# Performance work log

Measured on AMD Instinct MI355X. Metric: run time of the kernel, lower is better.

Reference implementation:

```python
import jax, jax.numpy as jnp
import numpy as np

N = 20000          # num nodes
DEG = 8            # directed avg degree before symmetrization
IN_C, HID, OUT_C, K = 128, 32, 16, 2


def _build_graph(n, deg, seed=0):
    """Build symmetric 1-hop A1 (no self loops) and exact 2-hop A2 edge lists,
    with D^{-1/2} A D^{-1/2} normalized values (mirrors _prepare_prop)."""
    rng = np.random.default_rng(seed)
    e = n * deg
    row = rng.integers(0, n, e)
    col = rng.integers(0, n, e)
    r = np.concatenate([row, col])
    c = np.concatenate([col, row])
    m = r != c
    keys1 = np.unique(r[m].astype(np.int64) * n + c[m])  # A1 = indicator(A - I)
    r1 = (keys1 // n).astype(np.int64)
    c1 = (keys1 % n).astype(np.int64)
    # exact 2-hop: nonzeros of A1@A1, minus A1 and diagonal
    degs = np.bincount(r1, minlength=n)
    indptr = np.concatenate([np.zeros(1, np.int64), np.cumsum(degs)])
    counts = degs[c1]                       # per edge (u,v): deg(v)
    cum = np.cumsum(counts)
    total = int(cum[-1])
    offs = np.arange(total) - np.repeat(cum - counts, counts)
    dst2 = c1[np.repeat(indptr[c1], counts) + offs]
    src2 = np.repeat(r1, counts)
    keys2 = np.unique(src2 * n + dst2)
    diag = np.arange(n, dtype=np.int64) * (n + 1)
    keys2 = np.setdiff1d(keys2, np.concatenate([keys1, diag]), assume_unique=True)
    r2 = (keys2 // n).astype(np.int64)
    c2 = (keys2 % n).astype(np.int64)

    def norm(rr, cc):  # D^{-1/2} A D^{-1/2} on binary symmetric adjacency
        d = np.bincount(rr, minlength=n).astype(np.float64)
        dis = np.where(d > 0, 1.0 / np.sqrt(np.maximum(d, 1.0)), 0.0)
        return (dis[rr] * dis[cc]).astype(np.float32)

    return r1, c1, norm(r1, c1), r2, c2, norm(r2, c2)


def setup_inputs() -> dict:
    key = jax.random.key(0)
    k1, k2, k3 = jax.random.split(key, 3)
    x = jax.random.normal(k1, (N, IN_C), dtype=jnp.float32)
    # xavier_uniform for the two dense weights
    ae = float(np.sqrt(6.0 / (IN_C + HID)))
    cdim = (2 ** (K + 1) - 1) * HID  # 224
    ac = float(np.sqrt(6.0 / (cdim + OUT_C)))
    w_embed = jax.random.uniform(k2, (IN_C, HID), jnp.float32, -ae, ae)
    w_classify = jax.random.uniform(k3, (cdim, OUT_C), jnp.float32, -ac, ac)
    r1, c1, v1, r2, c2, v2 = _build_graph(N, DEG)
    return {
        "x": x, "w_embed": w_embed, "w_classify": w_classify,
        "a1_row": jnp.asarray(r1), "a1_col": jnp.asarray(c1), "a1_val": jnp.asarray(v1),
        "a2_row": jnp.asarray(r2), "a2_col": jnp.asarray(c2), "a2_val": jnp.asarray(v2),
    }


def _spmm(row, col, val, x, n):
    # sparse @ dense: gather source rows, scale, scatter-add into dest rows
    return jax.ops.segment_sum(x[col] * val[:, None], row, num_segments=n)


def reference(x, w_embed, w_classify, a1_row, a1_col, a1_val, a2_row, a2_col, a2_val):
    n = x.shape[0]
    rs = [jax.nn.relu(x @ w_embed)]  # [N, HID]
    for _ in range(K):
        r = rs[-1]
        r1 = _spmm(a1_row, a1_col, a1_val, r, n)
        r2 = _spmm(a2_row, a2_col, a2_val, r, n)
        rs.append(jax.nn.relu(jnp.concatenate([r1, r2], axis=1)))
    r_final = jnp.concatenate(rs, axis=1)  # [N, 7*HID]; dropout is identity in eval
    return r_final @ w_classify            # [N, OUT_C]
```

## Files before the change

### kernel.cpp

```cpp
#include <hip/hip_runtime.h>

typedef unsigned int uint;
typedef unsigned short ushort;

#define IN_C 128
#define HID  32

__device__ __forceinline__ float bf_lo(uint u) { return __uint_as_float(u << 16); }
__device__ __forceinline__ float bf_hi(uint u) { return __uint_as_float(u & 0xffff0000u); }
__device__ __forceinline__ uint  f2bf(float f) {
    uint u = __float_as_uint(f);
    return (u + 0x7fffu + ((u >> 16) & 1u)) >> 16;
}

__global__ void embed_kernel(const float* __restrict__ x,
                             const float* __restrict__ w,
                             ushort* __restrict__ r0, int n) {
    __shared__ float wl[IN_C * HID];
    const int tid = threadIdx.x;
    for (int i = tid; i < IN_C * HID; i += blockDim.x) wl[i] = w[i];
    __syncthreads();
    const int row = blockIdx.x * 16 + tid / 16;
    const int h0  = (tid % 16) * 2;
    if (row >= n) return;
    const float4* xr = (const float4*)(x + (size_t)row * IN_C);
    float a0 = 0.f, a1 = 0.f;
#pragma unroll
    for (int k4 = 0; k4 < IN_C / 4; ++k4) {
        float4 xv = xr[k4];
        a0 += xv.x * wl[(4*k4+0)*HID + h0];     a1 += xv.x * wl[(4*k4+0)*HID + h0+1];
        a0 += xv.y * wl[(4*k4+1)*HID + h0];     a1 += xv.y * wl[(4*k4+1)*HID + h0+1];
        a0 += xv.z * wl[(4*k4+2)*HID + h0];     a1 += xv.z * wl[(4*k4+2)*HID + h0+1];
        a0 += xv.w * wl[(4*k4+3)*HID + h0];     a1 += xv.w * wl[(4*k4+3)*HID + h0+1];
    }
    uint p = f2bf(fmaxf(a0, 0.f)) | (f2bf(fmaxf(a1, 0.f)) << 16);
    ((uint*)r0)[(size_t)row * 16 + (tid % 16)] = p;
}

__global__ void build_indptr2(const int* __restrict__ r1, int E1, int* __restrict__ ip1,
                              const int* __restrict__ r2, int E2, int* __restrict__ ip2,
                              int n) {
    const int i = blockIdx.x * blockDim.x + threadIdx.x;
    if (i > n) return;
    int lo = 0, hi = E1;
    while (lo < hi) { int m = (lo + hi) >> 1; if (r1[m] < i) lo = m + 1; else hi = m; }
    ip1[i] = lo;
    lo = 0; hi = E2;
    while (lo < hi) { int m = (lo + hi) >> 1; if (r2[m] < i) lo = m + 1; else hi = m; }
    ip2[i] = lo;
}

template <int C>
__global__ __launch_bounds__(256) void spmm_level(
        const int* __restrict__ ip1, const int* __restrict__ col1,
        const float* __restrict__ val1,
        const int* __restrict__ ip2, const int* __restrict__ col2,
        const float* __restrict__ val2,
        const ushort* __restrict__ xin, ushort* __restrict__ out,
        int n, int nb1) {
    constexpr int L = C / 8;
    constexpr int W = 64 / L;
    const int lane = threadIdx.x & 63;
    const int wave = threadIdx.x >> 6;

    int bid = blockIdx.x;
    const int* ip; const int* col; const float* val; int off;
    if (bid >= nb1) { bid -= nb1; ip = ip2; col = col2; val = val2; off = C; }
    else            {             ip = ip1; col = col1; val = val1; off = 0; }

    const int row = bid * 4 + wave;
    if (row >= n) return;

    const int fl  = lane % L;
    const int way = lane / L;
    const ushort* xbase = xin + fl * 8;

    float acc[8];
#pragma unroll
    for (int j = 0; j < 8; ++j) acc[j] = 0.f;

    const int s = ip[row];
    const int e = ip[row + 1];
    int sv = (s + 3) & ~3;
    if (sv > e) sv = e;
    const int nv = (e - sv) / (4 * W);

    auto edge = [&](int c, float v) {
        const uint4 u = *(const uint4*)(xbase + (size_t)c * C);
        acc[0] += v * bf_lo(u.x);  acc[1] += v * bf_hi(u.x);
        acc[2] += v * bf_lo(u.y);  acc[3] += v * bf_hi(u.y);
        acc[4] += v * bf_lo(u.z);  acc[5] += v * bf_hi(u.z);
        acc[6] += v * bf_lo(u.w);  acc[7] += v * bf_hi(u.w);
    };

    for (int idx = s + way; idx < sv; idx += W) edge(col[idx], val[idx]);
    for (int i = 0; i < nv; ++i) {
        const int base = sv + (i * W + way) * 4;
        const int4   cc = *(const int4*)  (col + base);
        const float4 vv = *(const float4*)(val + base);
        edge(cc.x, vv.x); edge(cc.y, vv.y); edge(cc.z, vv.z); edge(cc.w, vv.w);
    }
    for (int idx = sv + nv * 4 * W + way; idx < e; idx += W) edge(col[idx], val[idx]);

#pragma unroll
    for (int m = L; m < 64; m <<= 1)
#pragma unroll
        for (int j = 0; j < 8; ++j) acc[j] += __shfl_xor(acc[j], m, 64);

    if (way == 0) {
        uint4 p;
        p.x = f2bf(fmaxf(acc[0], 0.f)) | (f2bf(fmaxf(acc[1], 0.f)) << 16);
        p.y = f2bf(fmaxf(acc[2], 0.f)) | (f2bf(fmaxf(acc[3], 0.f)) << 16);
        p.z = f2bf(fmaxf(acc[4], 0.f)) | (f2bf(fmaxf(acc[5], 0.f)) << 16);
        p.w = f2bf(fmaxf(acc[6], 0.f)) | (f2bf(fmaxf(acc[7], 0.f)) << 16);
        *(uint4*)(out + (size_t)row * (2 * C) + off + fl * 8) = p;
    }
}

#define CDIM 224
#define OUT_C 16
__global__ void classify_kernel(const ushort* __restrict__ r0,
                                const ushort* __restrict__ r1,
                                const ushort* __restrict__ r2,
                                const float* __restrict__ w,
                                float* __restrict__ out, int n) {
    __shared__ float wl[CDIM * OUT_C];
    const int tid = threadIdx.x;
    for (int i = tid; i < CDIM * OUT_C; i += blockDim.x) wl[i] = w[i];
    __syncthreads();
    const int row = blockIdx.x * 16 + tid / 16;
    const int o   = tid % 16;
    if (row >= n) return;
    float acc = 0.f;

    const uint4* a = (const uint4*)(r0 + (size_t)row * 32);
#pragma unroll
    for (int q = 0; q < 4; ++q) {
        uint4 u = a[q]; int j = q * 8;
        acc += bf_lo(u.x) * wl[(j+0)*OUT_C + o];  acc += bf_hi(u.x) * wl[(j+1)*OUT_C + o];
        acc += bf_lo(u.y) * wl[(j+2)*OUT_C + o];  acc += bf_hi(u.y) * wl[(j+3)*OUT_C + o];
        acc += bf_lo(u.z) * wl[(j+4)*OUT_C + o];  acc += bf_hi(u.z) * wl[(j+5)*OUT_C + o];
        acc += bf_lo(u.w) * wl[(j+6)*OUT_C + o];  acc += bf_hi(u.w) * wl[(j+7)*OUT_C + o];
    }
    const uint4* b = (const uint4*)(r1 + (size_t)row * 64);
#pragma unroll
    for (int q = 0; q < 8; ++q) {
        uint4 u = b[q]; int j = 32 + q * 8;
        acc += bf_lo(u.x) * wl[(j+0)*OUT_C + o];  acc += bf_hi(u.x) * wl[(j+1)*OUT_C + o];
        acc += bf_lo(u.y) * wl[(j+2)*OUT_C + o];  acc += bf_hi(u.y) * wl[(j+3)*OUT_C + o];
        acc += bf_lo(u.z) * wl[(j+4)*OUT_C + o];  acc += bf_hi(u.z) * wl[(j+5)*OUT_C + o];
        acc += bf_lo(u.w) * wl[(j+6)*OUT_C + o];  acc += bf_hi(u.w) * wl[(j+7)*OUT_C + o];
    }
    const uint4* c = (const uint4*)(r2 + (size_t)row * 128);
#pragma unroll
    for (int q = 0; q < 16; ++q) {
        uint4 u = c[q]; int j = 96 + q * 8;
        acc += bf_lo(u.x) * wl[(j+0)*OUT_C + o];  acc += bf_hi(u.x) * wl[(j+1)*OUT_C + o];
        acc += bf_lo(u.y) * wl[(j+2)*OUT_C + o];  acc += bf_hi(u.y) * wl[(j+3)*OUT_C + o];
        acc += bf_lo(u.z) * wl[(j+4)*OUT_C + o];  acc += bf_hi(u.z) * wl[(j+5)*OUT_C + o];
        acc += bf_lo(u.w) * wl[(j+6)*OUT_C + o];  acc += bf_hi(u.w) * wl[(j+7)*OUT_C + o];
    }
    out[(size_t)row * OUT_C + o] = acc;
}

extern "C" void kernel_launch(void* const* d_in, const int* in_sizes, int n_in,
                              void* d_out, int out_size, void* d_ws, size_t ws_size,
                              hipStream_t stream) {
    const float* x   = (const float*)d_in[0];
    const float* we  = (const float*)d_in[1];
    const float* wc  = (const float*)d_in[2];
    const int*   a1r = (const int*)  d_in[3];
    const int*   a1c = (const int*)  d_in[4];
    const float* a1v = (const float*)d_in[5];
    const int*   a2r = (const int*)  d_in[6];
    const int*   a2c = (const int*)  d_in[7];
    const float* a2v = (const float*)d_in[8];
    float* out = (float*)d_out;

    const int E1 = in_sizes[3];
    const int E2 = in_sizes[6];
    const int n  = in_sizes[0] / IN_C;

    ushort* r0 = (ushort*)d_ws;
    ushort* r1 = r0 + (size_t)n * 32;
    ushort* r2 = r1 + (size_t)n * 64;
    int*   ip1 = (int*)(r2 + (size_t)n * 128);
    int*   ip2 = ip1 + (n + 1);

    embed_kernel<<<(n + 15) / 16, 256, 0, stream>>>(x, we, r0, n);

    build_indptr2<<<(n + 256) / 256, 256, 0, stream>>>(a1r, E1, ip1, a2r, E2, ip2, n);

    const int nb = (n + 3) / 4;

    spmm_level<32><<<2 * nb, 256, 0, stream>>>(ip1, a1c, a1v, ip2, a2c, a2v,
                                               r0, r1, n, nb);
    spmm_level<64><<<2 * nb, 256, 0, stream>>>(ip1, a1c, a1v, ip2, a2c, a2v,
                                               r1, r2, n, nb);

    classify_kernel<<<(n + 15) / 16, 256, 0, stream>>>(r0, r1, r2, wc, out, n);
}
```

Before: 236.7 us.

## Merge embed and indptr kernels, software-pipeline SpMM gathers, pack two rows per wave

Fuses the embedding GEMM and the CSR indptr binary search into one launch by splitting blocks by index. The SpMM kernel gains a ROWS parameter so the 32-channel level processes two rows per wavefront. Its vectorized edge loop is software-pipelined, prefetching col/val quads two iterations ahead and issuing gathers one iteration ahead to hide latency. Block ordering is also swapped so the larger 2-hop blocks are scheduled first. This costs more registers and adds prologue and epilogue complexity.

```diff
diff --git a/kernel.cpp b/kernel.cpp
--- a/kernel.cpp
+++ b/kernel.cpp
@@ -13,106 +13,131 @@
     return (u + 0x7fffu + ((u >> 16) & 1u)) >> 16;
 }
 
-__global__ void embed_kernel(const float* __restrict__ x,
-                             const float* __restrict__ w,
-                             ushort* __restrict__ r0, int n) {
+__global__ void prep_kernel(const float* __restrict__ x,
+                            const float* __restrict__ w,
+                            ushort* __restrict__ r0,
+                            const int* __restrict__ a1r, int E1, int* __restrict__ ip1,
+                            const int* __restrict__ a2r, int E2, int* __restrict__ ip2,
+                            int n, int nbE) {
     __shared__ float wl[IN_C * HID];
     const int tid = threadIdx.x;
-    for (int i = tid; i < IN_C * HID; i += blockDim.x) wl[i] = w[i];
-    __syncthreads();
-    const int row = blockIdx.x * 16 + tid / 16;
-    const int h0  = (tid % 16) * 2;
-    if (row >= n) return;
-    const float4* xr = (const float4*)(x + (size_t)row * IN_C);
-    float a0 = 0.f, a1 = 0.f;
-#pragma unroll
-    for (int k4 = 0; k4 < IN_C / 4; ++k4) {
-        float4 xv = xr[k4];
-        a0 += xv.x * wl[(4*k4+0)*HID + h0];     a1 += xv.x * wl[(4*k4+0)*HID + h0+1];
-        a0 += xv.y * wl[(4*k4+1)*HID + h0];     a1 += xv.y * wl[(4*k4+1)*HID + h0+1];
-        a0 += xv.z * wl[(4*k4+2)*HID + h0];     a1 += xv.z * wl[(4*k4+2)*HID + h0+1];
-        a0 += xv.w * wl[(4*k4+3)*HID + h0];     a1 += xv.w * wl[(4*k4+3)*HID + h0+1];
-    }
-    uint p = f2bf(fmaxf(a0, 0.f)) | (f2bf(fmaxf(a1, 0.f)) << 16);
-    ((uint*)r0)[(size_t)row * 16 + (tid % 16)] = p;
-}
-
-__global__ void build_indptr2(const int* __restrict__ r1, int E1, int* __restrict__ ip1,
-                              const int* __restrict__ r2, int E2, int* __restrict__ ip2,
-                              int n) {
-    const int i = blockIdx.x * blockDim.x + threadIdx.x;
-    if (i > n) return;
-    int lo = 0, hi = E1;
-    while (lo < hi) { int m = (lo + hi) >> 1; if (r1[m] < i) lo = m + 1; else hi = m; }
-    ip1[i] = lo;
-    lo = 0; hi = E2;
-    while (lo < hi) { int m = (lo + hi) >> 1; if (r2[m] < i) lo = m + 1; else hi = m; }
-    ip2[i] = lo;
-}
-
-template <int C>
+    if (blockIdx.x < nbE) {
+        for (int i = tid; i < IN_C * HID; i += blockDim.x) wl[i] = w[i];
+        __syncthreads();
+        const int row = blockIdx.x * 16 + tid / 16;
+        const int h0  = (tid % 16) * 2;
+        if (row >= n) return;
+        const float4* xr = (const float4*)(x + (size_t)row * IN_C);
+        float a0 = 0.f, a1 = 0.f;
+#pragma unroll
+        for (int k4 = 0; k4 < IN_C / 4; ++k4) {
+            float4 xv = xr[k4];
+            a0 += xv.x * wl[(4*k4+0)*HID + h0];  a1 += xv.x * wl[(4*k4+0)*HID + h0+1];
+            a0 += xv.y * wl[(4*k4+1)*HID + h0];  a1 += xv.y * wl[(4*k4+1)*HID + h0+1];
+            a0 += xv.z * wl[(4*k4+2)*HID + h0];  a1 += xv.z * wl[(4*k4+2)*HID + h0+1];
+            a0 += xv.w * wl[(4*k4+3)*HID + h0];  a1 += xv.w * wl[(4*k4+3)*HID + h0+1];
+        }
+        uint p = f2bf(fmaxf(a0, 0.f)) | (f2bf(fmaxf(a1, 0.f)) << 16);
+        ((uint*)r0)[(size_t)row * 16 + (tid % 16)] = p;
+    } else {
+        const int i = (blockIdx.x - nbE) * 256 + tid;
+        if (i > n) return;
+        int lo = 0, hi = E1;
+        while (lo < hi) { int m = (lo + hi) >> 1; if (a1r[m] < i) lo = m + 1; else hi = m; }
+        ip1[i] = lo;
+        lo = 0; hi = E2;
+        while (lo < hi) { int m = (lo + hi) >> 1; if (a2r[m] < i) lo = m + 1; else hi = m; }
+        ip2[i] = lo;
+    }
+}
+
+template <int C, int ROWS>
 __global__ __launch_bounds__(256) void spmm_level(
         const int* __restrict__ ip1, const int* __restrict__ col1,
         const float* __restrict__ val1,
         const int* __restrict__ ip2, const int* __restrict__ col2,
         const float* __restrict__ val2,
         const ushort* __restrict__ xin, ushort* __restrict__ out,
-        int n, int nb1) {
-    constexpr int L = C / 8;
-    constexpr int W = 64 / L;
+        int n, int nb2) {
+    constexpr int L    = C / 8;
+    constexpr int SUBL = 64 / ROWS;
+    constexpr int W    = SUBL / L;
     const int lane = threadIdx.x & 63;
     const int wave = threadIdx.x >> 6;
+    const int sub  = lane / SUBL;
+    const int li   = lane % SUBL;
+    const int fl   = li % L;
+    const int way  = li / L;
 
     int bid = blockIdx.x;
     const int* ip; const int* col; const float* val; int off;
-    if (bid >= nb1) { bid -= nb1; ip = ip2; col = col2; val = val2; off = C; }
-    else            {             ip = ip1; col = col1; val = val1; off = 0; }
-
-    const int row = bid * 4 + wave;
+    if (bid < nb2) {             ip = ip2; col = col2; val = val2; off = C; }
+    else           { bid -= nb2; ip = ip1; col = col1; val = val1; off = 0; }
+
+    const int row = (bid * 4 + wave) * ROWS + sub;
     if (row >= n) return;
 
-    const int fl  = lane % L;
-    const int way = lane / L;
     const ushort* xbase = xin + fl * 8;
-
     float acc[8];
 #pragma unroll
     for (int j = 0; j < 8; ++j) acc[j] = 0.f;
+
+    auto gat = [&](int c) -> uint4 {
+        return *(const uint4*)(xbase + (size_t)c * C);
+    };
+    auto fmadd = [&](const uint4& u, float v) {
+        acc[0] += v * bf_lo(u.x); acc[1] += v * bf_hi(u.x);
+        acc[2] += v * bf_lo(u.y); acc[3] += v * bf_hi(u.y);
+        acc[4] += v * bf_lo(u.z); acc[5] += v * bf_hi(u.z);
+        acc[6] += v * bf_lo(u.w); acc[7] += v * bf_hi(u.w);
+    };
 
     const int s = ip[row];
     const int e = ip[row + 1];
-    int sv = (s + 3) & ~3;
-    if (sv > e) sv = e;
+    int sv = (s + 3) & ~3; if (sv > e) sv = e;
     const int nv = (e - sv) / (4 * W);
 
-    auto edge = [&](int c, float v) {
-        const uint4 u = *(const uint4*)(xbase + (size_t)c * C);
-        acc[0] += v * bf_lo(u.x);  acc[1] += v * bf_hi(u.x);
-        acc[2] += v * bf_lo(u.y);  acc[3] += v * bf_hi(u.y);
-        acc[4] += v * bf_lo(u.z);  acc[5] += v * bf_hi(u.z);
-        acc[6] += v * bf_lo(u.w);  acc[7] += v * bf_hi(u.w);
-    };
-
-    for (int idx = s + way; idx < sv; idx += W) edge(col[idx], val[idx]);
-    for (int i = 0; i < nv; ++i) {
-        const int base = sv + (i * W + way) * 4;
-        const int4   cc = *(const int4*)  (col + base);
-        const float4 vv = *(const float4*)(val + base);
-        edge(cc.x, vv.x); edge(cc.y, vv.y); edge(cc.z, vv.z); edge(cc.w, vv.w);
-    }
-    for (int idx = sv + nv * 4 * W + way; idx < e; idx += W) edge(col[idx], val[idx]);
-
-#pragma unroll
-    for (int m = L; m < 64; m <<= 1)
+    for (int idx = s + way; idx < sv; idx += W) fmadd(gat(col[idx]), val[idx]);
+
+    const int4*   cp = (const int4*)  (col + sv) + way;
+    const float4* vp = (const float4*)(val + sv) + way;
+    int4 ccA, ccB; float4 vvA, vvB, vcur;
+    uint4 g0, g1, g2, g3;
+    if (nv > 0) {
+        ccA = cp[0]; vvA = vp[0];
+        g0 = gat(ccA.x); g1 = gat(ccA.y); g2 = gat(ccA.z); g3 = gat(ccA.w);
+        vcur = vvA;
+        if (nv > 1) { ccA = cp[W];     vvA = vp[W]; }
+        if (nv > 2) { ccB = cp[2 * W]; vvB = vp[2 * W]; }
+        else        { ccB = ccA;       vvB = vvA; }
+    }
+    for (int i = 0; i + 1 < nv; ++i) {
+        uint4 h0 = gat(ccA.x), h1 = gat(ccA.y), h2 = gat(ccA.z), h3 = gat(ccA.w);
+        float4 vnxt = vvA;
+        ccA = ccB; vvA = vvB;
+        const int pidx = (i + 3 < nv) ? (i + 3) : (nv - 1);
+        ccB = cp[pidx * W]; vvB = vp[pidx * W];
+        fmadd(g0, vcur.x); fmadd(g1, vcur.y); fmadd(g2, vcur.z); fmadd(g3, vcur.w);
+        g0 = h0; g1 = h1; g2 = h2; g3 = h3; vcur = vnxt;
+    }
+    if (nv > 0) {
+        fmadd(g0, vcur.x); fmadd(g1, vcur.y); fmadd(g2, vcur.z); fmadd(g3, vcur.w);
+    }
+
+    for (int idx = sv + nv * 4 * W + way; idx < e; idx += W)
+        fmadd(gat(col[idx]), val[idx]);
+
+#pragma unroll
+    for (int m = L; m < SUBL; m <<= 1)
 #pragma unroll
         for (int j = 0; j < 8; ++j) acc[j] += __shfl_xor(acc[j], m, 64);
 
     if (way == 0) {
         uint4 p;
-        p.x = f2bf(fmaxf(acc[0], 0.f)) | (f2bf(fmaxf(acc[1], 0.f)) << 16);
-        p.y = f2bf(fmaxf(acc[2], 0.f)) | (f2bf(fmaxf(acc[3], 0.f)) << 16);
-        p.z = f2bf(fmaxf(acc[4], 0.f)) | (f2bf(fmaxf(acc[5], 0.f)) << 16);
-        p.w = f2bf(fmaxf(acc[6], 0.f)) | (f2bf(fmaxf(acc[7], 0.f)) << 16);
+        p.x = f2bf(fmaxf(acc[0],0.f)) | (f2bf(fmaxf(acc[1],0.f)) << 16);
+        p.y = f2bf(fmaxf(acc[2],0.f)) | (f2bf(fmaxf(acc[3],0.f)) << 16);
+        p.z = f2bf(fmaxf(acc[4],0.f)) | (f2bf(fmaxf(acc[5],0.f)) << 16);
+        p.w = f2bf(fmaxf(acc[6],0.f)) | (f2bf(fmaxf(acc[7],0.f)) << 16);
         *(uint4*)(out + (size_t)row * (2 * C) + off + fl * 8) = p;
     }
 }
@@ -187,16 +212,23 @@
     int*   ip1 = (int*)(r2 + (size_t)n * 128);
     int*   ip2 = ip1 + (n + 1);
 
-    embed_kernel<<<(n + 15) / 16, 256, 0, stream>>>(x, we, r0, n);
-
-    build_indptr2<<<(n + 256) / 256, 256, 0, stream>>>(a1r, E1, ip1, a2r, E2, ip2, n);
-
-    const int nb = (n + 3) / 4;
-
-    spmm_level<32><<<2 * nb, 256, 0, stream>>>(ip1, a1c, a1v, ip2, a2c, a2v,
-                                               r0, r1, n, nb);
-    spmm_level<64><<<2 * nb, 256, 0, stream>>>(ip1, a1c, a1v, ip2, a2c, a2v,
-                                               r1, r2, n, nb);
+    {
+        const int nbE = (n + 15) / 16;
+        const int nbI = (n + 1 + 255) / 256;
+        prep_kernel<<<nbE + nbI, 256, 0, stream>>>(x, we, r0, a1r, E1, ip1,
+                                                   a2r, E2, ip2, n, nbE);
+    }
+
+    {
+        const int nb = (n + 7) / 8;
+        spmm_level<32, 2><<<2 * nb, 256, 0, stream>>>(ip1, a1c, a1v, ip2, a2c, a2v,
+                                                      r0, r1, n, nb);
+    }
+    {
+        const int nb = (n + 3) / 4;
+        spmm_level<64, 1><<<2 * nb, 256, 0, stream>>>(ip1, a1c, a1v, ip2, a2c, a2v,
+                                                      r1, r2, n, nb);
+    }
 
     classify_kernel<<<(n + 15) / 16, 256, 0, stream>>>(r0, r1, r2, wc, out, n);
 }
```

New measurement: 236.0 us. Within noise of the previous version (-0.3%).
